# Kernel optimization log

Measured on AMD Instinct MI355X. Metric: run time of the kernel, lower is better.

## Reference

```python
import jax, jax.numpy as jnp
import numpy as np


def setup_inputs() -> dict:
    key = jax.random.key(0)
    k1, k2, k3, k4, k5 = jax.random.split(key, 5)
    B, L1, L2, H = 16, 1024, 1024, 1024
    x = jax.random.normal(k1, (B, L1, H), dtype=jnp.float32)
    y = jax.random.normal(k2, (B, L2, H), dtype=jnp.float32)
    y_mask = jax.random.randint(k3, (B, L2), 0, 2) > 0  # True = masked out
    W = jax.random.normal(k4, (H, H), dtype=jnp.float32) * (1.0 / np.sqrt(H))
    b = jax.random.normal(k5, (H,), dtype=jnp.float32) * 0.01
    return {"x": x, "y": y, "y_mask": y_mask, "W": W, "b": b}


def reference(x, y, y_mask, W, b):
    # shared linear projection + ReLU (nn.Linear: v @ W.T + b)
    x_proj = jax.nn.relu(jnp.einsum("blh,dh->bld", x, W) + b)  # [B, L1, H]
    y_proj = jax.nn.relu(jnp.einsum("bmh,dh->bmd", y, W) + b)  # [B, L2, H]
    # unscaled attention scores [B, L1, L2]
    scores = jnp.einsum("bld,bmd->blm", x_proj, y_proj)
    scores = jnp.where(y_mask[:, None, :], -jnp.inf, scores)
    alpha = jax.nn.softmax(scores, axis=-1)
    # weighted sum over original (unprojected) y values
    matched_seq = jnp.einsum("blm,bmh->blh", alpha, y)
    return matched_seq
```

## Files before the change

### kernel.cpp

```cpp
#include <hip/hip_runtime.h>
#include <hip/hip_fp16.h>

typedef _Float16 f16;
typedef _Float16 half4 __attribute__((ext_vector_type(4)));
typedef _Float16 half8 __attribute__((ext_vector_type(8)));
typedef float f32x4 __attribute__((ext_vector_type(4)));

#define BATCH 16
#define L 1024
#define H 1024

__global__ __launch_bounds__(256) void cvt_wx(const float* __restrict__ W,
                                              f16* __restrict__ Wh,
                                              const float* __restrict__ x,
                                              f16* __restrict__ Xh) {
  const float* src;
  f16* dst;
  long i;
  if (blockIdx.x < 512) {
    src = W; dst = Wh;
    i = (long)blockIdx.x * 2048 + threadIdx.x * 8;
  } else {
    src = x; dst = Xh;
    i = ((long)blockIdx.x - 512) * 2048 + threadIdx.x * 8;
  }
  const float4 a = *(const float4*)(&src[i]);
  const float4 b = *(const float4*)(&src[i + 4]);
  half8 h;
  h[0] = (f16)a.x; h[1] = (f16)a.y; h[2] = (f16)a.z; h[3] = (f16)a.w;
  h[4] = (f16)b.x; h[5] = (f16)b.y; h[6] = (f16)b.z; h[7] = (f16)b.w;
  *(half8*)(&dst[i]) = h;
}

__global__ __launch_bounds__(256) void transpose_y(const float* __restrict__ Y,
                                                   f16* __restrict__ Yh,
                                                   f16* __restrict__ Yt) {
  __shared__ f16 tile[64][36];
  const int b = blockIdx.z;
  const float* Yb = Y + (long)b * L * H;
  f16* Yhb = Yh + (long)b * L * H;
  f16* Ytb = Yt + (long)b * L * H;
  const int h0 = blockIdx.x * 64, m0 = blockIdx.y * 32;
  const int tid = threadIdx.x;

  const int hc = (tid & 15) * 4;
  #pragma unroll
  for (int rr = 0; rr < 2; ++rr) {
    const int m = (tid >> 4) + rr * 16;
    const float4 v = *(const float4*)(&Yb[(long)(m0 + m) * H + h0 + hc]);
    half4 h4;
    h4[0] = (f16)v.x; h4[1] = (f16)v.y; h4[2] = (f16)v.z; h4[3] = (f16)v.w;
    *(half4*)(&Yhb[(long)(m0 + m) * H + h0 + hc]) = h4;
    tile[hc + 0][m] = h4[0];
    tile[hc + 1][m] = h4[1];
    tile[hc + 2][m] = h4[2];
    tile[hc + 3][m] = h4[3];
  }
  __syncthreads();
  const int m4 = (tid & 7) * 4;
  #pragma unroll
  for (int it = 0; it < 2; ++it) {
    const int hh = (tid >> 3) + it * 32;
    *(half4*)(&Ytb[(long)(h0 + hh) * L + m0 + m4]) =
        *(const half4*)(&tile[hh][m4]);
  }
}

#define GLD16(g, l)                                           \
  __builtin_amdgcn_global_load_lds(                           \
      (const __attribute__((address_space(1))) void*)(g),     \
      (__attribute__((address_space(3))) void*)(l), 16, 0, 0)

template <int EPI, int TAG>
__global__ __launch_bounds__(512, 4) void gemm128(
    const f16* __restrict__ Ap, const f16* __restrict__ Bp,
    const float* __restrict__ bias, void* __restrict__ Cp,
    long sA, long sB, long sC, int nxyShift) {
  __shared__ f16 lds[3 * 12288];
  constexpr int N = 1024, K = 1024, NT = 32;

  const int tid = threadIdx.x;
  const int lane = tid & 63;
  const int wid = tid >> 6;
  const int wm = wid >> 1;
  const int wn = wid & 1;

  const int nwg = gridDim.x;
  const int orig = blockIdx.x;
  const int wg = (orig & 7) * (nwg >> 3) + (orig >> 3);
  const int bz = wg >> nxyShift;
  const int rxy = wg & ((1 << nxyShift) - 1);
  const int bx = rxy & 7;
  const int by = rxy >> 3;
  const int row0 = by * 256, col0 = bx * 128;

  const f16* A = Ap + (long)bz * sA;
  const f16* B = Bp + (long)bz * sB;

  const int srow = lane >> 2;
  const int sslot = (lane & 3) ^ ((lane >> 3) & 3);
  const f16* gA0 = A + (long)(row0 + wid * 32 + srow) * K + sslot * 8;
  const f16* gA1 = A + (long)(row0 + wid * 32 + 16 + srow) * K + sslot * 8;
  const f16* gB0 = B + (long)(col0 + wid * 16 + srow) * K + sslot * 8;
  char* ldsw = (char*)lds;

  const int fr = lane & 15, fq = lane >> 4;
  const int rsw = (fq ^ ((fr >> 1) & 3)) << 4;
  const int aByte = (wm * 64 + fr) * 64 + rsw;
  const int bByte = (wn * 64 + fr) * 64 + rsw;
  const char* ldsr = (const char*)lds;

  f32x4 acc[4][4];
  #pragma unroll
  for (int i = 0; i < 4; ++i)
    #pragma unroll
    for (int j = 0; j < 4; ++j)
      acc[i][j] = (f32x4){0.f, 0.f, 0.f, 0.f};

  #pragma unroll
  for (int p = 0; p < 2; ++p) {
    char* sb = ldsw + p * 24576;
    GLD16(gA0, sb + wid * 2048);
    GLD16(gA1, sb + wid * 2048 + 1024);
    GLD16(gB0, sb + 16384 + wid * 1024);
    gA0 += 32; gA1 += 32; gB0 += 32;
  }
  asm volatile("s_waitcnt vmcnt(3)" ::: "memory");
  __builtin_amdgcn_s_barrier();
  __builtin_amdgcn_sched_barrier(0);

  int cb = 0, pb = 2 * 24576;
  for (int t = 0; t < NT; ++t) {
    if (t + 2 < NT) {
      char* sb = ldsw + pb;
      GLD16(gA0, sb + wid * 2048);
      GLD16(gA1, sb + wid * 2048 + 1024);
      GLD16(gB0, sb + 16384 + wid * 1024);
      gA0 += 32; gA1 += 32; gB0 += 32;
    }
    const char* base = ldsr + cb;
    half8 av[4], bv[4];
    #pragma unroll
    for (int j = 0; j < 4; ++j)
      bv[j] = *(const half8*)(base + 16384 + bByte + j * 1024);
    #pragma unroll
    for (int i = 0; i < 4; ++i)
      av[i] = *(const half8*)(base + aByte + i * 1024);
    __builtin_amdgcn_s_setprio(1);
    #pragma unroll
    for (int i = 0; i < 4; ++i)
      #pragma unroll
      for (int j = 0; j < 4; ++j)
        acc[i][j] = __builtin_amdgcn_mfma_f32_16x16x32_f16(av[i], bv[j],
                                                           acc[i][j], 0, 0, 0);
    __builtin_amdgcn_s_setprio(0);
    if (t < NT - 1) {
      __builtin_amdgcn_sched_barrier(0);
      if (t <= NT - 3)
        asm volatile("s_waitcnt vmcnt(3)" ::: "memory");
      else
        asm volatile("s_waitcnt vmcnt(0)" ::: "memory");
      __builtin_amdgcn_s_barrier();
      __builtin_amdgcn_sched_barrier(0);
      cb = (cb == 49152) ? 0 : cb + 24576;
      pb = (pb == 49152) ? 0 : pb + 24576;
    }
  }

  if (EPI == 0) {
    f16* C = (f16*)Cp + (long)bz * sC;
    #pragma unroll
    for (int j = 0; j < 4; ++j) {
      const int col = col0 + wn * 64 + j * 16 + fr;
      const float bvs = bias[col];
      #pragma unroll
      for (int i = 0; i < 4; ++i) {
        const int rowb = row0 + wm * 64 + i * 16 + fq * 4;
        #pragma unroll
        for (int r = 0; r < 4; ++r) {
          float v = acc[i][j][r] + bvs;
          v = v > 0.f ? v : 0.f;
          C[(long)(rowb + r) * N + col] = (f16)v;
        }
      }
    }
  } else {
    float* C = (float*)Cp + (long)bz * sC;
    #pragma unroll
    for (int j = 0; j < 4; ++j) {
      const int col = col0 + wn * 64 + j * 16 + fr;
      #pragma unroll
      for (int i = 0; i < 4; ++i) {
        const int rowb = row0 + wm * 64 + i * 16 + fq * 4;
        #pragma unroll
        for (int r = 0; r < 4; ++r)
          C[(long)(rowb + r) * N + col] = acc[i][j][r];
      }
    }
  }
}

__global__ __launch_bounds__(256) void softmax_rows(const float* __restrict__ S,
                                                    const int* __restrict__ mask,
                                                    f16* __restrict__ P) {
  const int b = blockIdx.y;
  const int l = blockIdx.x;
  const float* srow = S + ((long)b * L + l) * L;
  f16* prow = P + ((long)b * L + l) * L;
  const int* mrow = mask + b * L;
  const int t = threadIdx.x;

  const float4 v = *(const float4*)(&srow[t * 4]);
  const int4 mk = *(const int4*)(&mrow[t * 4]);
  const float x0 = mk.x ? -1e30f : v.x;
  const float x1 = mk.y ? -1e30f : v.y;
  const float x2 = mk.z ? -1e30f : v.z;
  const float x3 = mk.w ? -1e30f : v.w;

  float mx = fmaxf(fmaxf(x0, x1), fmaxf(x2, x3));
  #pragma unroll
  for (int off = 32; off >= 1; off >>= 1)
    mx = fmaxf(mx, __shfl_xor(mx, off));
  __shared__ float red[8];
  const int wid = t >> 6, lane = t & 63;
  if (lane == 0) red[wid] = mx;
  __syncthreads();
  mx = fmaxf(fmaxf(red[0], red[1]), fmaxf(red[2], red[3]));

  const float e0 = __expf(x0 - mx), e1 = __expf(x1 - mx);
  const float e2 = __expf(x2 - mx), e3 = __expf(x3 - mx);
  float s = e0 + e1 + e2 + e3;
  #pragma unroll
  for (int off = 32; off >= 1; off >>= 1)
    s += __shfl_xor(s, off);
  if (lane == 0) red[4 + wid] = s;
  __syncthreads();
  s = red[4] + red[5] + red[6] + red[7];
  const float inv = 1.f / s;
  half4 h;
  h[0] = (f16)(e0 * inv); h[1] = (f16)(e1 * inv);
  h[2] = (f16)(e2 * inv); h[3] = (f16)(e3 * inv);
  *(half4*)(&prow[t * 4]) = h;
}

extern "C" void kernel_launch(void* const* d_in, const int* in_sizes, int n_in,
                              void* d_out, int out_size, void* d_ws,
                              size_t ws_size, hipStream_t stream) {
  const float* x = (const float*)d_in[0];
  const float* y = (const float*)d_in[1];
  const int* ymask = (const int*)d_in[2];
  const float* W = (const float*)d_in[3];
  const float* bias = (const float*)d_in[4];
  float* out = (float*)d_out;

  char* ws = (char*)d_ws;
  f16* Wh = (f16*)(ws);
  f16* Yt = (f16*)(ws + (1L << 21));
  f16* XYp = (f16*)(ws + (1L << 21) + (1L << 25));
  f16* XYh = (f16*)(ws + (1L << 21) + (1L << 25) + (1L << 26));
  float* Sc = (float*)XYh;
  f16* Alpha = XYp;

  f16* Xh = XYh;
  f16* Yh = XYh + (long)BATCH * L * H;

  cvt_wx<<<512 + 8192, 256, 0, stream>>>(W, Wh, x, Xh);
  transpose_y<<<dim3(16, 32, BATCH), 256, 0, stream>>>(y, Yh, Yt);

  gemm128<0, 0><<<1024, 512, 0, stream>>>(XYh, Wh, bias, XYp, 0, 0, 0, 10);

  gemm128<1, 1><<<512, 512, 0, stream>>>(XYp, XYp + (long)BATCH * L * H,
                                         nullptr, Sc, (long)L * H, (long)L * H,
                                         (long)L * L, 5);

  softmax_rows<<<dim3(L, BATCH), 256, 0, stream>>>(Sc, ymask, Alpha);

  gemm128<1, 2><<<512, 512, 0, stream>>>(Alpha, Yt, nullptr, out, (long)L * L,
                                         (long)H * L, (long)L * H, 5);
}
```

Measured before the change: 224.8 us.

## Compact unmasked y rows to skip masked keys across projection, scores and PV

Adds a mask scan that computes prefix positions of unmasked y rows. The y projection then gathers only those rows, the score GEMM and softmax cover only the compacted key count (padded to 32), and the final alpha·y GEMM shortens its K loop to match. With a random mask about half the keys are masked, so the y-side projection, score and PV work all shrink. The cost is extra small kernels, a scattered transpose write and data-dependent grid early exits.

```diff
diff --git a/kernel.cpp b/kernel.cpp
--- a/kernel.cpp
+++ b/kernel.cpp
@@ -32,17 +32,75 @@
   *(half8*)(&dst[i]) = h;
 }
 
+__global__ __launch_bounds__(256) void mask_scan(const int* __restrict__ mask,
+                                                 int* __restrict__ posx,
+                                                 int* __restrict__ midxg,
+                                                 int* __restrict__ cntA) {
+  const int b = blockIdx.x;
+  const int t = threadIdx.x;
+  const int4 mk = *(const int4*)(&mask[b * 1024 + t * 4]);
+  const int f0 = (mk.x == 0), f1 = (mk.y == 0);
+  const int f2 = (mk.z == 0), f3 = (mk.w == 0);
+  const int s = f0 + f1 + f2 + f3;
+  int v = s;
+  const int lane = t & 63, wd = t >> 6;
+  #pragma unroll
+  for (int off = 1; off < 64; off <<= 1) {
+    const int u = __shfl_up(v, off);
+    if (lane >= off) v += u;
+  }
+  __shared__ int wsum[4];
+  if (lane == 63) wsum[wd] = v;
+  __syncthreads();
+  int wb = 0;
+  #pragma unroll
+  for (int k = 0; k < 3; ++k)
+    if (k < wd) wb += wsum[k];
+  int e = wb + v - s;
+  const int base = b * 1024 + t * 4;
+  posx[base + 0] = e;
+  if (f0) midxg[b * 1024 + e] = t * 4 + 0;
+  e += f0;
+  posx[base + 1] = e;
+  if (f1) midxg[b * 1024 + e] = t * 4 + 1;
+  e += f1;
+  posx[base + 2] = e;
+  if (f2) midxg[b * 1024 + e] = t * 4 + 2;
+  e += f2;
+  posx[base + 3] = e;
+  if (f3) midxg[b * 1024 + e] = t * 4 + 3;
+  e += f3;
+  if (t == 255) cntA[b] = e;
+}
+
+__global__ void offsets_k(const int* __restrict__ cntA, int* __restrict__ off17) {
+  if (threadIdx.x == 0) {
+    int a = 0;
+    off17[0] = 0;
+    for (int b = 0; b < 16; ++b) { a += cntA[b]; off17[b + 1] = a; }
+  }
+}
+
 __global__ __launch_bounds__(256) void transpose_y(const float* __restrict__ Y,
+                                                   const int* __restrict__ mask,
+                                                   const int* __restrict__ posx,
+                                                   const int* __restrict__ cntA,
                                                    f16* __restrict__ Yh,
-                                                   f16* __restrict__ Yt) {
+                                                   f16* __restrict__ Ytc) {
   __shared__ f16 tile[64][36];
+  __shared__ int jcol[32];
+  __shared__ int jval[32];
   const int b = blockIdx.z;
   const float* Yb = Y + (long)b * L * H;
   f16* Yhb = Yh + (long)b * L * H;
-  f16* Ytb = Yt + (long)b * L * H;
+  f16* Ytb = Ytc + (long)b * L * H;
   const int h0 = blockIdx.x * 64, m0 = blockIdx.y * 32;
   const int tid = threadIdx.x;
 
+  if (tid < 32) {
+    jcol[tid] = posx[b * 1024 + m0 + tid];
+    jval[tid] = (mask[b * 1024 + m0 + tid] == 0);
+  }
   const int hc = (tid & 15) * 4;
   #pragma unroll
   for (int rr = 0; rr < 2; ++rr) {
@@ -57,12 +115,21 @@
     tile[hc + 3][m] = h4[3];
   }
   __syncthreads();
-  const int m4 = (tid & 7) * 4;
-  #pragma unroll
-  for (int it = 0; it < 2; ++it) {
-    const int hh = (tid >> 3) + it * 32;
-    *(half4*)(&Ytb[(long)(h0 + hh) * L + m0 + m4]) =
-        *(const half4*)(&tile[hh][m4]);
+  const int hh = tid >> 2;
+  const int mg = (tid & 3) * 8;
+  #pragma unroll
+  for (int i = 0; i < 8; ++i) {
+    const int m = mg + i;
+    if (jval[m])
+      Ytb[(long)(h0 + hh) * L + jcol[m]] = tile[hh][m];
+  }
+  if (m0 == L - 32) {
+    const int cnt = cntA[b];
+    const int jend = (cnt + 31) & ~31;
+    const int jz = cnt + (tid & 31);
+    if (jz < jend)
+      for (int r = tid >> 5; r < 64; r += 8)
+        Ytb[(long)(h0 + r) * L + jz] = (f16)0.f;
   }
 }
 
@@ -71,13 +138,27 @@
       (const __attribute__((address_space(1))) void*)(g),     \
       (__attribute__((address_space(3))) void*)(l), 16, 0, 0)
 
-template <int EPI, int TAG>
+__device__ __forceinline__ long gather_row(int r, const int* __restrict__ o17,
+                                           const int* __restrict__ midxg,
+                                           int total) {
+  if (r < 16384) return r;
+  int g = r - 16384;
+  if (g >= total) g = total - 1;
+  int b = 0;
+  #pragma unroll
+  for (int k = 1; k <= 16; ++k) b += (g >= o17[k]);
+  const int m = midxg[b * 1024 + g - o17[b]];
+  return 16384L + b * 1024 + m;
+}
+
+template <int MODE>
 __global__ __launch_bounds__(512, 4) void gemm128(
     const f16* __restrict__ Ap, const f16* __restrict__ Bp,
     const float* __restrict__ bias, void* __restrict__ Cp,
-    long sA, long sB, long sC, int nxyShift) {
+    const int* __restrict__ off17, const int* __restrict__ midxg,
+    int nxyShift) {
   __shared__ f16 lds[3 * 12288];
-  constexpr int N = 1024, K = 1024, NT = 32;
+  constexpr int N = 1024, K = 1024;
 
   const int tid = threadIdx.x;
   const int lane = tid & 63;
@@ -94,14 +175,35 @@
   const int by = rxy >> 3;
   const int row0 = by * 256, col0 = bx * 128;
 
-  const f16* A = Ap + (long)bz * sA;
-  const f16* B = Bp + (long)bz * sB;
-
   const int srow = lane >> 2;
   const int sslot = (lane & 3) ^ ((lane >> 3) & 3);
-  const f16* gA0 = A + (long)(row0 + wid * 32 + srow) * K + sslot * 8;
-  const f16* gA1 = A + (long)(row0 + wid * 32 + 16 + srow) * K + sslot * 8;
-  const f16* gB0 = B + (long)(col0 + wid * 16 + srow) * K + sslot * 8;
+
+  int nt = 32;
+  const f16 *gA0, *gA1, *gB0;
+  if (MODE == 0) {
+    const int total = off17[16];
+    if (row0 >= 16384 + total) return;
+    gA0 = Ap + gather_row(row0 + wid * 32 + srow, off17, midxg, total) * K +
+          sslot * 8;
+    gA1 = Ap + gather_row(row0 + wid * 32 + 16 + srow, off17, midxg, total) * K +
+          sslot * 8;
+    gB0 = Bp + (long)(col0 + wid * 16 + srow) * K + sslot * 8;
+  } else if (MODE == 1) {
+    const int cnt = off17[bz + 1] - off17[bz];
+    if (col0 >= ((cnt + 31) & ~31)) return;
+    gA0 = Ap + (long)(bz * 1024 + row0 + wid * 32 + srow) * K + sslot * 8;
+    gA1 = gA0 + 16L * K;
+    gB0 = Ap + (long)(16384 + off17[bz] + col0 + wid * 16 + srow) * K +
+          sslot * 8;
+  } else {
+    const int cnt = off17[bz + 1] - off17[bz];
+    nt = ((cnt + 31) & ~31) >> 5;
+    gA0 = Ap + (long)bz * (1 << 20) +
+          (long)(row0 + wid * 32 + srow) * 1024 + sslot * 8;
+    gA1 = gA0 + 16L * 1024;
+    gB0 = Bp + (long)bz * (1 << 20) +
+          (long)(col0 + wid * 16 + srow) * 1024 + sslot * 8;
+  }
   char* ldsw = (char*)lds;
 
   const int fr = lane & 15, fq = lane >> 4;
@@ -130,6 +232,7 @@
   __builtin_amdgcn_sched_barrier(0);
 
   int cb = 0, pb = 2 * 24576;
+  const int NT = (MODE == 2) ? nt : 32;
   for (int t = 0; t < NT; ++t) {
     if (t + 2 < NT) {
       char* sb = ldsw + pb;
@@ -167,8 +270,8 @@
     }
   }
 
-  if (EPI == 0) {
-    f16* C = (f16*)Cp + (long)bz * sC;
+  if (MODE == 0) {
+    f16* C = (f16*)Cp;
     #pragma unroll
     for (int j = 0; j < 4; ++j) {
       const int col = col0 + wn * 64 + j * 16 + fr;
@@ -185,7 +288,7 @@
       }
     }
   } else {
-    float* C = (float*)Cp + (long)bz * sC;
+    float* C = (float*)Cp + (long)bz * (1 << 20);
     #pragma unroll
     for (int j = 0; j < 4; ++j) {
       const int col = col0 + wn * 64 + j * 16 + fr;
@@ -201,29 +304,30 @@
 }
 
 __global__ __launch_bounds__(256) void softmax_rows(const float* __restrict__ S,
-                                                    const int* __restrict__ mask,
+                                                    const int* __restrict__ off17,
                                                     f16* __restrict__ P) {
   const int b = blockIdx.y;
   const int l = blockIdx.x;
+  const int t = threadIdx.x;
+  const int cnt = off17[b + 1] - off17[b];
+  const int cnt32 = (cnt + 31) & ~31;
   const float* srow = S + ((long)b * L + l) * L;
   f16* prow = P + ((long)b * L + l) * L;
-  const int* mrow = mask + b * L;
-  const int t = threadIdx.x;
 
   const float4 v = *(const float4*)(&srow[t * 4]);
-  const int4 mk = *(const int4*)(&mrow[t * 4]);
-  const float x0 = mk.x ? -1e30f : v.x;
-  const float x1 = mk.y ? -1e30f : v.y;
-  const float x2 = mk.z ? -1e30f : v.z;
-  const float x3 = mk.w ? -1e30f : v.w;
+  const int j0 = t * 4;
+  const float x0 = (j0 + 0 < cnt) ? v.x : -1e30f;
+  const float x1 = (j0 + 1 < cnt) ? v.y : -1e30f;
+  const float x2 = (j0 + 2 < cnt) ? v.z : -1e30f;
+  const float x3 = (j0 + 3 < cnt) ? v.w : -1e30f;
 
   float mx = fmaxf(fmaxf(x0, x1), fmaxf(x2, x3));
   #pragma unroll
   for (int off = 32; off >= 1; off >>= 1)
     mx = fmaxf(mx, __shfl_xor(mx, off));
   __shared__ float red[8];
-  const int wid = t >> 6, lane = t & 63;
-  if (lane == 0) red[wid] = mx;
+  const int wd = t >> 6, lane = t & 63;
+  if (lane == 0) red[wd] = mx;
   __syncthreads();
   mx = fmaxf(fmaxf(red[0], red[1]), fmaxf(red[2], red[3]));
 
@@ -233,14 +337,16 @@
   #pragma unroll
   for (int off = 32; off >= 1; off >>= 1)
     s += __shfl_xor(s, off);
-  if (lane == 0) red[4 + wid] = s;
+  if (lane == 0) red[4 + wd] = s;
   __syncthreads();
   s = red[4] + red[5] + red[6] + red[7];
   const float inv = 1.f / s;
-  half4 h;
-  h[0] = (f16)(e0 * inv); h[1] = (f16)(e1 * inv);
-  h[2] = (f16)(e2 * inv); h[3] = (f16)(e3 * inv);
-  *(half4*)(&prow[t * 4]) = h;
+  if (j0 < cnt32) {
+    half4 h;
+    h[0] = (f16)(e0 * inv); h[1] = (f16)(e1 * inv);
+    h[2] = (f16)(e2 * inv); h[3] = (f16)(e3 * inv);
+    *(half4*)(&prow[j0]) = h;
+  }
 }
 
 extern "C" void kernel_launch(void* const* d_in, const int* in_sizes, int n_in,
@@ -255,26 +361,34 @@
 
   char* ws = (char*)d_ws;
   f16* Wh = (f16*)(ws);
-  f16* Yt = (f16*)(ws + (1L << 21));
+  f16* Ytc = (f16*)(ws + (1L << 21));
   f16* XYp = (f16*)(ws + (1L << 21) + (1L << 25));
   f16* XYh = (f16*)(ws + (1L << 21) + (1L << 25) + (1L << 26));
   float* Sc = (float*)XYh;
   f16* Alpha = XYp;
 
+  char* meta = (char*)XYp + 60L * (1 << 20);
+  int* posx = (int*)meta;
+  int* midxg = (int*)(meta + (1 << 16));
+  int* cntA = (int*)(meta + (1 << 17));
+  int* off17 = (int*)(meta + (1 << 17) + 256);
+
   f16* Xh = XYh;
   f16* Yh = XYh + (long)BATCH * L * H;
 
   cvt_wx<<<512 + 8192, 256, 0, stream>>>(W, Wh, x, Xh);
-  transpose_y<<<dim3(16, 32, BATCH), 256, 0, stream>>>(y, Yh, Yt);
-
-  gemm128<0, 0><<<1024, 512, 0, stream>>>(XYh, Wh, bias, XYp, 0, 0, 0, 10);
-
-  gemm128<1, 1><<<512, 512, 0, stream>>>(XYp, XYp + (long)BATCH * L * H,
-                                         nullptr, Sc, (long)L * H, (long)L * H,
-                                         (long)L * L, 5);
-
-  softmax_rows<<<dim3(L, BATCH), 256, 0, stream>>>(Sc, ymask, Alpha);
-
-  gemm128<1, 2><<<512, 512, 0, stream>>>(Alpha, Yt, nullptr, out, (long)L * L,
-                                         (long)H * L, (long)L * H, 5);
-}
+  mask_scan<<<16, 256, 0, stream>>>(ymask, posx, midxg, cntA);
+  offsets_k<<<1, 64, 0, stream>>>(cntA, off17);
+  transpose_y<<<dim3(16, 32, BATCH), 256, 0, stream>>>(y, ymask, posx, cntA,
+                                                       Yh, Ytc);
+
+  gemm128<0><<<1024, 512, 0, stream>>>(XYh, Wh, bias, XYp, off17, midxg, 10);
+
+  gemm128<1><<<512, 512, 0, stream>>>(XYp, nullptr, nullptr, Sc, off17, midxg,
+                                      5);
+
+  softmax_rows<<<dim3(L, BATCH), 256, 0, stream>>>(Sc, off17, Alpha);
+
+  gemm128<2><<<512, 512, 0, stream>>>(Alpha, Ytc, nullptr, out, off17, midxg,
+                                      5);
+}
```

New measurement: 220.1 us. -2.1%, faster.
